# Performance work log

Measured on AMD Instinct MI355X. Metric: run time of the kernel, lower is better.

## Reference

```python
import jax, jax.numpy as jnp
import numpy as np

B, S, D, H = 4, 2048, 1024, 16
HD = D // H
THETA = 10000.0


def rope(x, pos, theta=THETA):
    # x: [..., seq, d], pos: broadcastable to [..., seq]
    d = x.shape[-1]
    half = d // 2
    inv_freq = 1.0 / (theta ** (jnp.arange(half, dtype=jnp.float32) * 2.0 / d))  # [half]
    ang = pos[..., None].astype(jnp.float32) * inv_freq  # [..., seq, half]
    cos, sin = jnp.cos(ang), jnp.sin(ang)
    x1, x2 = x[..., 0::2], x[..., 1::2]
    r1 = x1 * cos - x2 * sin
    r2 = x1 * sin + x2 * cos
    return jnp.stack([r1, r2], axis=-1).reshape(x.shape).astype(x.dtype)


def setup_inputs() -> dict:
    key = jax.random.key(0)
    ks = jax.random.split(key, 5)
    x = jax.random.normal(ks[0], (B, S, D), dtype=jnp.float32)
    token_positions = jnp.tile(jnp.arange(S, dtype=jnp.int64 if jax.config.jax_enable_x64 else jnp.int32), (B, 1))
    scale = 0.02
    Wq = jax.random.normal(ks[1], (D, D), dtype=jnp.float32) * scale
    Wk = jax.random.normal(ks[2], (D, D), dtype=jnp.float32) * scale
    Wv = jax.random.normal(ks[3], (D, D), dtype=jnp.float32) * scale
    Wo = jax.random.normal(ks[4], (D, D), dtype=jnp.float32) * scale
    return {"x": x, "token_positions": token_positions, "Wq": Wq, "Wk": Wk, "Wv": Wv, "Wo": Wo}


def reference(x, token_positions, Wq, Wk, Wv, Wo):
    b, s, d = x.shape
    # QKV projections (torch Linear: x @ W.T), split heads -> [b, h, s, hd]
    def proj(W):
        y = jnp.einsum('bsd,ed->bse', x, W)
        return y.reshape(b, s, H, HD).transpose(0, 2, 1, 3)
    Q, K, V = proj(Wq), proj(Wk), proj(Wv)
    # token_positions [..., seq] -> [..., 1, seq] to broadcast over heads
    pos = token_positions[:, None, :]  # [b, 1, s]
    Q = rope(Q, pos)
    K = rope(K, pos)
    # causal mask and scaled dot-product attention
    idx = jnp.arange(s)
    causal = idx[:, None] >= idx[None, :]  # [s, s], query >= key
    scores = jnp.einsum('bhqd,bhkd->bhqk', Q, K) / jnp.sqrt(jnp.float32(HD))
    scores = jnp.where(causal, scores, -jnp.inf)
    weights = jax.nn.softmax(scores, axis=-1)
    o = jnp.einsum('bhqk,bhkd->bhqd', weights, V)
    o = o.transpose(0, 2, 1, 3).reshape(b, s, d)  # merge heads
    return jnp.einsum('bsd,ed->bse', o, Wo)
```

## Files before the change

kernel.cpp:

```cpp
#include <hip/hip_runtime.h>

#define S_LEN 2048
#define NH 16
#define HDIM 64
#define DMODEL 1024

typedef __attribute__((ext_vector_type(8))) short bf16x8;
typedef __attribute__((ext_vector_type(4))) float f32x4;

__device__ __forceinline__ short f2bf(float f) {
    union { float f; unsigned u; } x; x.f = f;
    unsigned r = x.u + 0x7fffu + ((x.u >> 16) & 1u);
    return (short)(r >> 16);
}

#define GLDS(g, l) __builtin_amdgcn_global_load_lds( \
    (__attribute__((address_space(1))) void*)(g),    \
    (__attribute__((address_space(3))) void*)(l), 16, 0, 0)

#define QSCALE 0.18033688011112042f
#define FREQ_L 0.41524101186109327f

__global__ __launch_bounds__(256) void prep(const float* __restrict__ x,
                                            const float* __restrict__ wq,
                                            const float* __restrict__ wk,
                                            const float* __restrict__ wv,
                                            const float* __restrict__ wo,
                                            const int* __restrict__ tp,
                                            short* __restrict__ xb,
                                            short* __restrict__ wqb,
                                            short* __restrict__ wkb,
                                            short* __restrict__ wvb,
                                            short* __restrict__ wob,
                                            float2* __restrict__ tab) {
    int bid = blockIdx.x;
    if (bid < 8192) {
        int i = bid * 256 + threadIdx.x;
        float4 v = ((const float4*)x)[i];
        short4 o;
        o.x = f2bf(v.x); o.y = f2bf(v.y); o.z = f2bf(v.z); o.w = f2bf(v.w);
        ((short4*)xb)[i] = o;
    } else if (bid < 12288) {
        int sel = (bid - 8192) >> 10;
        const float* in = sel == 0 ? wq : sel == 1 ? wk : sel == 2 ? wv : wo;
        short* out = sel == 0 ? wqb : sel == 1 ? wkb : sel == 2 ? wvb : wob;
        int i = ((bid - 8192) & 1023) * 256 + threadIdx.x;
        float4 v = ((const float4*)in)[i];
        short4 o;
        o.x = f2bf(v.x); o.y = f2bf(v.y); o.z = f2bf(v.z); o.w = f2bf(v.w);
        ((short4*)out)[i] = o;
    } else {
        int idx = (bid - 12288) * 256 + threadIdx.x;
        int b = idx >> 16, s = (idx >> 5) & 2047, i = idx & 31;
        float p = (float)tp[(b << 11) + s];
        float freq = exp2f(-(float)i * FREQ_L);
        float sn, cs;
        sincosf(p * freq, &sn, &cs);
        tab[idx] = make_float2(cs, sn);
    }
}

__global__ __launch_bounds__(256) void gemm_qkv(const short* __restrict__ A,
                                                const short* __restrict__ Bq,
                                                const short* __restrict__ Bk,
                                                const short* __restrict__ Bv,
                                                const float2* __restrict__ tab,
                                                short* __restrict__ Qo,
                                                short* __restrict__ Ko,
                                                short* __restrict__ Vo) {
    constexpr int K = 1024, BK = 64;
    __shared__ __align__(16) short sa[128 * BK];
    __shared__ __align__(16) short sb[128 * BK];

    const int sel = blockIdx.x >> 3;
    const int bn = blockIdx.x & 7;
    const int bm = blockIdx.y;
    const short* Bm = sel == 0 ? Bq : sel == 1 ? Bk : Bv;
    short* Cb = sel == 0 ? Qo : sel == 1 ? Ko : Vo;

    const int tid = threadIdx.x;
    const int lane = tid & 63;
    const int w = tid >> 6;
    const int wm = w >> 1, wn = w & 1;
    const int quad = lane >> 4, l16 = lane & 15;
    const int l7 = l16 & 7;

    int aoff[4], boff[4];
#pragma unroll
    for (int i = 0; i < 4; i++) {
        int Lc = i * 256 + tid;
        int row = Lc >> 3;
        int cc = (Lc & 7) ^ (row & 7);
        aoff[i] = (bm * 128 + row) * K + cc * 8;
        boff[i] = (bn * 128 + row) * K + cc * 8;
    }

    f32x4 acc[4][4] = {};

    for (int k0 = 0; k0 < K; k0 += BK) {
#pragma unroll
        for (int i = 0; i < 4; i++)
            GLDS(A + aoff[i] + k0, (char*)sa + i * 4096 + w * 1024);
#pragma unroll
        for (int i = 0; i < 4; i++)
            GLDS(Bm + boff[i] + k0, (char*)sb + i * 4096 + w * 1024);
        __syncthreads();

#pragma unroll
        for (int kc = 0; kc < 2; kc++) {
            const int c = ((kc * 4 + quad) ^ l7) * 8;
            bf16x8 af[4], bfm[4];
#pragma unroll
            for (int mi = 0; mi < 4; mi++)
                af[mi] = *(const bf16x8*)&sa[(wm * 64 + mi * 16 + l16) * BK + c];
#pragma unroll
            for (int ni = 0; ni < 4; ni++)
                bfm[ni] = *(const bf16x8*)&sb[(wn * 64 + ni * 16 + l16) * BK + c];
#pragma unroll
            for (int mi = 0; mi < 4; mi++)
#pragma unroll
                for (int ni = 0; ni < 4; ni++)
                    acc[mi][ni] = __builtin_amdgcn_mfma_f32_16x16x32_bf16(af[mi], bfm[ni],
                                                                          acc[mi][ni], 0, 0, 0);
        }
        __syncthreads();
    }

    const int gm0 = bm * 128 + wm * 64;
    const int gn0 = bn * 128 + wn * 64;

    if (sel == 2) {
#pragma unroll
        for (int mi = 0; mi < 4; mi++)
#pragma unroll
            for (int ni = 0; ni < 4; ni++)
#pragma unroll
                for (int r = 0; r < 4; r++) {
                    int gm = gm0 + mi * 16 + quad * 4 + r;
                    int gn = gn0 + ni * 16 + l16;
                    int b = gm >> 11, s = gm & 2047;
                    int h = gn >> 6,  hd = gn & 63;
                    Cb[((b * NH + h) * HDIM + hd) * S_LEN + s] = f2bf(acc[mi][ni][r]);
                }
    } else {
        const float qs = (sel == 0) ? QSCALE : 1.0f;
#pragma unroll
        for (int mi = 0; mi < 4; mi++)
#pragma unroll
            for (int r = 0; r < 4; r++) {
                int gm = gm0 + mi * 16 + quad * 4 + r;
                const float2* trow = tab + (gm << 5);
                int b = gm >> 11, s = gm & 2047;
#pragma unroll
                for (int ni = 0; ni < 4; ni++) {
                    float2 cs = trow[ni * 8 + (l16 >> 1)];
                    float v = acc[mi][ni][r];
                    float prt = __shfl_xor(v, 1, 64);
                    float val = (l16 & 1) ? (prt * cs.y + v * cs.x)
                                          : (v * cs.x - prt * cs.y);
                    int gn = gn0 + ni * 16 + l16;
                    int h = gn >> 6, hd = gn & 63;
                    Cb[((b * NH + h) * S_LEN + s) * HDIM + hd] = f2bf(val * qs);
                }
            }
    }
}

__global__ __launch_bounds__(256) void gemm_o(const short* __restrict__ A,
                                              const short* __restrict__ Bm,
                                              float* __restrict__ Cf) {
    constexpr int N = 1024, K = 1024, BK = 64;
    __shared__ __align__(16) short sa[128 * BK];
    __shared__ __align__(16) short sb[64 * BK];

    const int tid = threadIdx.x;
    const int lane = tid & 63;
    const int w = tid >> 6;
    const int quad = lane >> 4, l16 = lane & 15;
    const int l7 = l16 & 7;
    const int bn = blockIdx.x, bm = blockIdx.y;
    const int arow0 = bm * 128, brow0 = bn * 64;

    int aoff[4], boff[2];
#pragma unroll
    for (int i = 0; i < 4; i++) {
        int Lc = i * 256 + tid;
        int row = Lc >> 3;
        int cc = (Lc & 7) ^ (row & 7);
        aoff[i] = (arow0 + row) * K + cc * 8;
    }
#pragma unroll
    for (int i = 0; i < 2; i++) {
        int Lc = i * 256 + tid;
        int row = Lc >> 3;
        int cc = (Lc & 7) ^ (row & 7);
        boff[i] = (brow0 + row) * K + cc * 8;
    }

    f32x4 acc[2][4] = {};

    for (int k0 = 0; k0 < K; k0 += BK) {
#pragma unroll
        for (int i = 0; i < 4; i++)
            GLDS(A + aoff[i] + k0, (char*)sa + i * 4096 + w * 1024);
#pragma unroll
        for (int i = 0; i < 2; i++)
            GLDS(Bm + boff[i] + k0, (char*)sb + i * 4096 + w * 1024);
        __syncthreads();

#pragma unroll
        for (int kc = 0; kc < 2; kc++) {
            const int c = ((kc * 4 + quad) ^ l7) * 8;
            bf16x8 af[2], bfm[4];
#pragma unroll
            for (int mi = 0; mi < 2; mi++)
                af[mi] = *(const bf16x8*)&sa[(w * 32 + mi * 16 + l16) * BK + c];
#pragma unroll
            for (int ni = 0; ni < 4; ni++)
                bfm[ni] = *(const bf16x8*)&sb[(ni * 16 + l16) * BK + c];
#pragma unroll
            for (int mi = 0; mi < 2; mi++)
#pragma unroll
                for (int ni = 0; ni < 4; ni++)
                    acc[mi][ni] = __builtin_amdgcn_mfma_f32_16x16x32_bf16(af[mi], bfm[ni],
                                                                          acc[mi][ni], 0, 0, 0);
        }
        __syncthreads();
    }

    const int gm0 = arow0 + w * 32;
#pragma unroll
    for (int mi = 0; mi < 2; mi++)
#pragma unroll
        for (int ni = 0; ni < 4; ni++)
#pragma unroll
            for (int r = 0; r < 4; r++) {
                int gm = gm0 + mi * 16 + quad * 4 + r;
                int gn = brow0 + ni * 16 + l16;
                Cf[gm * N + gn] = acc[mi][ni][r];
            }
}

__global__ __launch_bounds__(256, 3) void attn(const short* __restrict__ Q,
                                               const short* __restrict__ Km,
                                               const short* __restrict__ Vt,
                                               short* __restrict__ O) {
    __shared__ __align__(16) short kbuf[2][64 * 64];
    __shared__ __align__(16) short vbuf[2][64 * 64];
    __shared__ __align__(16) short pbuf[4][32 * 64];

    const int lane = threadIdx.x & 63;
    const int w = threadIdx.x >> 6;
    const int quad = lane >> 4, l16 = lane & 15;
    const int l7 = l16 & 7;
    const int bh = blockIdx.y;

    const short* Qg = Q  + bh * S_LEN * 64;
    const short* Kg = Km + bh * S_LEN * 64;
    const short* Vg = Vt + bh * 64 * S_LEN;
    short* myp = &pbuf[w][0];

    const int b = bh >> 4, h = bh & 15;

    bf16x8 ones;
#pragma unroll
    for (int j = 0; j < 8; j++) ones[j] = (short)0x3f80;

    auto stage = [&](int kt, int par) {
        const short* kt_base = Kg + kt * 64 * 64;
        const short* vt_base = Vg + kt * 64;
#pragma unroll
        for (int i = 0; i < 2; ++i) {
            int ch = w * 128 + i * 64 + lane;
            int row = ch >> 3;
            int c = (ch & 7) ^ (row & 7);
            GLDS(kt_base + row * 64 + c * 8, (char*)&kbuf[par][(w * 128 + i * 64) * 8]);
        }
#pragma unroll
        for (int i = 0; i < 2; ++i) {
            int ch = w * 128 + i * 64 + lane;
            int row = ch >> 3;
            int c = (ch & 7) ^ (row & 7);
            GLDS(vt_base + row * S_LEN + c * 8, (char*)&vbuf[par][(w * 128 + i * 64) * 8]);
        }
    };

    const int QtA = blockIdx.x;
    const int QtB = 15 - blockIdx.x;

    stage(0, 0);
    int t = 0;

    for (int phase = 0; phase < 2; ++phase) {
        const int Qt = phase ? QtB : QtA;
        const int nkt = 2 * Qt + 2;

        bf16x8 aq[2][2];
#pragma unroll
        for (int mi = 0; mi < 2; mi++) {
            int qrow = Qt * 128 + w * 32 + mi * 16 + l16;
#pragma unroll
            for (int kc = 0; kc < 2; kc++)
                aq[mi][kc] = *(const bf16x8*)&Qg[qrow * 64 + kc * 32 + quad * 8];
        }

        f32x4 oacc[2][4] = {};
        f32x4 lacc[2] = {};

        for (int kt = 0; kt < nkt; ++kt, ++t) {
            __syncthreads();
            if (kt + 1 < nkt)    stage(kt + 1, (t + 1) & 1);
            else if (phase == 0) stage(0,      (t + 1) & 1);
            const short* kb_cur = &kbuf[t & 1][0];
            const short* vb_cur = &vbuf[t & 1][0];

            f32x4 sc[2][4] = {};
#pragma unroll
            for (int nt = 0; nt < 4; nt++) {
                int raddr = (nt * 16 + l16) * 64;
#pragma unroll
                for (int kc = 0; kc < 2; kc++) {
                    bf16x8 kf = *(const bf16x8*)&kb_cur[raddr + (((quad + kc * 4) ^ l7) * 8)];
                    sc[0][nt] = __builtin_amdgcn_mfma_f32_16x16x32_bf16(aq[0][kc], kf, sc[0][nt], 0, 0, 0);
                    sc[1][nt] = __builtin_amdgcn_mfma_f32_16x16x32_bf16(aq[1][kc], kf, sc[1][nt], 0, 0, 0);
                }
            }
            if (kt >= nkt - 2) {
#pragma unroll
                for (int mi = 0; mi < 2; mi++)
#pragma unroll
                    for (int nt = 0; nt < 4; nt++)
#pragma unroll
                        for (int r = 0; r < 4; r++) {
                            int col = kt * 64 + nt * 16 + l16;
                            int row = Qt * 128 + w * 32 + mi * 16 + quad * 4 + r;
                            if (col > row) sc[mi][nt][r] = -__builtin_inff();
                        }
            }
#pragma unroll
            for (int mi = 0; mi < 2; mi++)
#pragma unroll
                for (int nt = 0; nt < 4; nt++)
#pragma unroll
                    for (int r = 0; r < 4; r++) {
                        float pv = __builtin_amdgcn_exp2f(sc[mi][nt][r]);
                        int q = mi * 16 + quad * 4 + r;
                        union { float f; unsigned short us[2]; } uu;
                        uu.f = pv;
                        myp[q * 64 + (((nt * 2 + (l16 >> 3)) ^ (q & 7)) * 8) + l7] =
                            (short)uu.us[1];
                    }
            bf16x8 ap[2][2];
#pragma unroll
            for (int mi = 0; mi < 2; mi++)
#pragma unroll
                for (int kc = 0; kc < 2; kc++)
                    ap[mi][kc] = *(const bf16x8*)&myp[(mi * 16 + l16) * 64 +
                                                      (((quad + kc * 4) ^ l7) * 8)];
#pragma unroll
            for (int nt = 0; nt < 4; nt++) {
                int raddr = (nt * 16 + l16) * 64;
#pragma unroll
                for (int kc = 0; kc < 2; kc++) {
                    bf16x8 vf = *(const bf16x8*)&vb_cur[raddr + (((quad + kc * 4) ^ l7) * 8)];
                    oacc[0][nt] = __builtin_amdgcn_mfma_f32_16x16x32_bf16(ap[0][kc], vf, oacc[0][nt], 0, 0, 0);
                    oacc[1][nt] = __builtin_amdgcn_mfma_f32_16x16x32_bf16(ap[1][kc], vf, oacc[1][nt], 0, 0, 0);
                }
            }
#pragma unroll
            for (int mi = 0; mi < 2; mi++) {
                lacc[mi] = __builtin_amdgcn_mfma_f32_16x16x32_bf16(ap[mi][0], ones, lacc[mi], 0, 0, 0);
                lacc[mi] = __builtin_amdgcn_mfma_f32_16x16x32_bf16(ap[mi][1], ones, lacc[mi], 0, 0, 0);
            }
        }
#pragma unroll
        for (int mi = 0; mi < 2; mi++)
#pragma unroll
            for (int r = 0; r < 4; r++) {
                float inv = 1.0f / lacc[mi][r];
                int srow = Qt * 128 + w * 32 + mi * 16 + quad * 4 + r;
#pragma unroll
                for (int nt = 0; nt < 4; nt++) {
                    int hd = nt * 16 + l16;
                    O[(b * S_LEN + srow) * DMODEL + h * HDIM + hd] = f2bf(oacc[mi][nt][r] * inv);
                }
            }
    }
}

extern "C" void kernel_launch(void* const* d_in, const int* in_sizes, int n_in,
                              void* d_out, int out_size, void* d_ws, size_t ws_size,
                              hipStream_t stream) {
    const float* x  = (const float*)d_in[0];
    const int*   tp = (const int*)d_in[1];
    const float* Wq = (const float*)d_in[2];
    const float* Wk = (const float*)d_in[3];
    const float* Wv = (const float*)d_in[4];
    const float* Wo = (const float*)d_in[5];
    float* out = (float*)d_out;

    char* ws = (char*)d_ws;
    const size_t MB = 1024 * 1024;
    short* xb  = (short*)(ws);
    short* wqb = (short*)(ws + 16 * MB);
    short* wkb = (short*)(ws + 18 * MB);
    short* wvb = (short*)(ws + 20 * MB);
    short* wob = (short*)(ws + 22 * MB);
    short* Qb  = (short*)(ws + 24 * MB);
    short* Kb  = (short*)(ws + 40 * MB);
    short* Vtb = (short*)(ws + 56 * MB);
    float2* tab = (float2*)d_out;

    prep<<<13312, 256, 0, stream>>>(x, Wq, Wk, Wv, Wo, tp,
                                    xb, wqb, wkb, wvb, wob, tab);

    gemm_qkv<<<dim3(24, 64), 256, 0, stream>>>(xb, wqb, wkb, wvb, tab, Qb, Kb, Vtb);

    attn<<<dim3(8, 64), 256, 0, stream>>>(Qb, Kb, Vtb, xb);

    gemm_o<<<dim3(16, 64), 256, 0, stream>>>(xb, wob, out);
}
```

Before: 279.4 us.

## Triple-buffer LDS in QKV and output-projection GEMMs with async prefetch pipeline

Both projection GEMMs switch from a single-buffered BK=64 loop with two __syncthreads per step to a three-stage ring of BK=32 LDS tiles. Global-to-LDS loads for tile k+2 are issued before computing tile k, and completion is tracked with explicit vmcnt waits and a single barrier per step. The LDS swizzle is adjusted for the narrower tile. This is meant to overlap global memory latency with MFMA work and halve the barriers per tile. The cost is more LDS per block and reliance on hand-tuned vmcnt counts for correctness.

New measurement: 276.0 us. About the same (-1.2%).

```diff
diff --git a/kernel.cpp b/kernel.cpp
--- a/kernel.cpp
+++ b/kernel.cpp
@@ -68,9 +68,9 @@
                                                 short* __restrict__ Qo,
                                                 short* __restrict__ Ko,
                                                 short* __restrict__ Vo) {
-    constexpr int K = 1024, BK = 64;
-    __shared__ __align__(16) short sa[128 * BK];
-    __shared__ __align__(16) short sb[128 * BK];
+    constexpr int K = 1024, BK = 32;
+    __shared__ __align__(16) short sa[3][128 * BK];
+    __shared__ __align__(16) short sb[3][128 * BK];
 
     const int sel = blockIdx.x >> 3;
     const int bn = blockIdx.x & 7;
@@ -83,48 +83,69 @@
     const int w = tid >> 6;
     const int wm = w >> 1, wn = w & 1;
     const int quad = lane >> 4, l16 = lane & 15;
-    const int l7 = l16 & 7;
-
-    int aoff[4], boff[4];
-#pragma unroll
-    for (int i = 0; i < 4; i++) {
-        int Lc = i * 256 + tid;
-        int row = Lc >> 3;
-        int cc = (Lc & 7) ^ (row & 7);
-        aoff[i] = (bm * 128 + row) * K + cc * 8;
-        boff[i] = (bn * 128 + row) * K + cc * 8;
-    }
+
+    int aoff[2], boff[2];
+#pragma unroll
+    for (int i = 0; i < 2; i++) {
+        int cs = i * 256 + tid;
+        int row = cs >> 2;
+        int gc = (cs & 3) ^ ((row >> 1) & 3);
+        aoff[i] = (bm * 128 + row) * K + gc * 8;
+        boff[i] = (bn * 128 + row) * K + gc * 8;
+    }
+
+    auto stage = [&](int kt, int b) {
+        const int k0 = kt * BK;
+#pragma unroll
+        for (int i = 0; i < 2; i++)
+            GLDS(A + aoff[i] + k0, (char*)&sa[b][0] + i * 4096 + w * 1024);
+#pragma unroll
+        for (int i = 0; i < 2; i++)
+            GLDS(Bm + boff[i] + k0, (char*)&sb[b][0] + i * 4096 + w * 1024);
+    };
 
     f32x4 acc[4][4] = {};
-
-    for (int k0 = 0; k0 < K; k0 += BK) {
-#pragma unroll
-        for (int i = 0; i < 4; i++)
-            GLDS(A + aoff[i] + k0, (char*)sa + i * 4096 + w * 1024);
-#pragma unroll
-        for (int i = 0; i < 4; i++)
-            GLDS(Bm + boff[i] + k0, (char*)sb + i * 4096 + w * 1024);
-        __syncthreads();
-
-#pragma unroll
-        for (int kc = 0; kc < 2; kc++) {
-            const int c = ((kc * 4 + quad) ^ l7) * 8;
-            bf16x8 af[4], bfm[4];
+    const int rsw = (quad ^ ((l16 >> 1) & 3)) * 8;
+
+    auto compute = [&](int b) {
+        bf16x8 af[4];
+#pragma unroll
+        for (int mi = 0; mi < 4; mi++)
+            af[mi] = *(const bf16x8*)&sa[b][(wm * 64 + mi * 16 + l16) * BK + rsw];
+#pragma unroll
+        for (int ni = 0; ni < 4; ni++) {
+            bf16x8 bfr = *(const bf16x8*)&sb[b][(wn * 64 + ni * 16 + l16) * BK + rsw];
 #pragma unroll
             for (int mi = 0; mi < 4; mi++)
-                af[mi] = *(const bf16x8*)&sa[(wm * 64 + mi * 16 + l16) * BK + c];
-#pragma unroll
-            for (int ni = 0; ni < 4; ni++)
-                bfm[ni] = *(const bf16x8*)&sb[(wn * 64 + ni * 16 + l16) * BK + c];
-#pragma unroll
-            for (int mi = 0; mi < 4; mi++)
-#pragma unroll
-                for (int ni = 0; ni < 4; ni++)
-                    acc[mi][ni] = __builtin_amdgcn_mfma_f32_16x16x32_bf16(af[mi], bfm[ni],
-                                                                          acc[mi][ni], 0, 0, 0);
-        }
-        __syncthreads();
-    }
+                acc[mi][ni] = __builtin_amdgcn_mfma_f32_16x16x32_bf16(af[mi], bfr,
+                                                                     acc[mi][ni], 0, 0, 0);
+        }
+    };
+
+    stage(0, 0);
+    stage(1, 1);
+
+    auto step = [&](int kt, int b, int bs) {
+        asm volatile("s_waitcnt vmcnt(4)" ::: "memory");
+        __builtin_amdgcn_s_barrier();
+        __builtin_amdgcn_sched_barrier(0);
+        stage(kt + 2, bs);
+        compute(b);
+    };
+
+    for (int kt = 0; kt < 30; kt += 3) {
+        step(kt + 0, 0, 2);
+        step(kt + 1, 1, 0);
+        step(kt + 2, 2, 1);
+    }
+    asm volatile("s_waitcnt vmcnt(4)" ::: "memory");
+    __builtin_amdgcn_s_barrier();
+    __builtin_amdgcn_sched_barrier(0);
+    compute(0);
+    asm volatile("s_waitcnt vmcnt(0)" ::: "memory");
+    __builtin_amdgcn_s_barrier();
+    __builtin_amdgcn_sched_barrier(0);
+    compute(1);
 
     const int gm0 = bm * 128 + wm * 64;
     const int gn0 = bn * 128 + wn * 64;
@@ -167,66 +188,83 @@
 }
 
 __global__ __launch_bounds__(256) void gemm_o(const short* __restrict__ A,
-                                              const short* __restrict__ Bm,
+                                              const short* __restrict__ Bw,
                                               float* __restrict__ Cf) {
-    constexpr int N = 1024, K = 1024, BK = 64;
-    __shared__ __align__(16) short sa[128 * BK];
-    __shared__ __align__(16) short sb[64 * BK];
+    constexpr int N = 1024, K = 1024, BK = 32;
+    __shared__ __align__(16) short sa[3][128 * BK];
+    __shared__ __align__(16) short sb[3][64 * BK];
 
     const int tid = threadIdx.x;
     const int lane = tid & 63;
     const int w = tid >> 6;
     const int quad = lane >> 4, l16 = lane & 15;
-    const int l7 = l16 & 7;
     const int bn = blockIdx.x, bm = blockIdx.y;
     const int arow0 = bm * 128, brow0 = bn * 64;
 
-    int aoff[4], boff[2];
-#pragma unroll
-    for (int i = 0; i < 4; i++) {
-        int Lc = i * 256 + tid;
-        int row = Lc >> 3;
-        int cc = (Lc & 7) ^ (row & 7);
-        aoff[i] = (arow0 + row) * K + cc * 8;
-    }
+    int aoff[2], boff;
 #pragma unroll
     for (int i = 0; i < 2; i++) {
-        int Lc = i * 256 + tid;
-        int row = Lc >> 3;
-        int cc = (Lc & 7) ^ (row & 7);
-        boff[i] = (brow0 + row) * K + cc * 8;
-    }
+        int cs = i * 256 + tid;
+        int row = cs >> 2;
+        int gc = (cs & 3) ^ ((row >> 1) & 3);
+        aoff[i] = (arow0 + row) * K + gc * 8;
+    }
+    {
+        int row = tid >> 2;
+        int gc = (tid & 3) ^ ((row >> 1) & 3);
+        boff = (brow0 + row) * K + gc * 8;
+    }
+
+    auto stage = [&](int kt, int b) {
+        const int k0 = kt * BK;
+#pragma unroll
+        for (int i = 0; i < 2; i++)
+            GLDS(A + aoff[i] + k0, (char*)&sa[b][0] + i * 4096 + w * 1024);
+        GLDS(Bw + boff + k0, (char*)&sb[b][0] + w * 1024);
+    };
 
     f32x4 acc[2][4] = {};
-
-    for (int k0 = 0; k0 < K; k0 += BK) {
-#pragma unroll
-        for (int i = 0; i < 4; i++)
-            GLDS(A + aoff[i] + k0, (char*)sa + i * 4096 + w * 1024);
-#pragma unroll
-        for (int i = 0; i < 2; i++)
-            GLDS(Bm + boff[i] + k0, (char*)sb + i * 4096 + w * 1024);
-        __syncthreads();
-
-#pragma unroll
-        for (int kc = 0; kc < 2; kc++) {
-            const int c = ((kc * 4 + quad) ^ l7) * 8;
-            bf16x8 af[2], bfm[4];
+    const int rsw = (quad ^ ((l16 >> 1) & 3)) * 8;
+
+    auto compute = [&](int b) {
+        bf16x8 af[2];
+#pragma unroll
+        for (int mi = 0; mi < 2; mi++)
+            af[mi] = *(const bf16x8*)&sa[b][(w * 32 + mi * 16 + l16) * BK + rsw];
+#pragma unroll
+        for (int ni = 0; ni < 4; ni++) {
+            bf16x8 bfr = *(const bf16x8*)&sb[b][(ni * 16 + l16) * BK + rsw];
 #pragma unroll
             for (int mi = 0; mi < 2; mi++)
-                af[mi] = *(const bf16x8*)&sa[(w * 32 + mi * 16 + l16) * BK + c];
-#pragma unroll
-            for (int ni = 0; ni < 4; ni++)
-                bfm[ni] = *(const bf16x8*)&sb[(ni * 16 + l16) * BK + c];
-#pragma unroll
-            for (int mi = 0; mi < 2; mi++)
-#pragma unroll
-                for (int ni = 0; ni < 4; ni++)
-                    acc[mi][ni] = __builtin_amdgcn_mfma_f32_16x16x32_bf16(af[mi], bfm[ni],
-                                                                          acc[mi][ni], 0, 0, 0);
-        }
-        __syncthreads();
-    }
+                acc[mi][ni] = __builtin_amdgcn_mfma_f32_16x16x32_bf16(af[mi], bfr,
+                                                                     acc[mi][ni], 0, 0, 0);
+        }
+    };
+
+    stage(0, 0);
+    stage(1, 1);
+
+    auto step = [&](int kt, int b, int bs) {
+        asm volatile("s_waitcnt vmcnt(3)" ::: "memory");
+        __builtin_amdgcn_s_barrier();
+        __builtin_amdgcn_sched_barrier(0);
+        stage(kt + 2, bs);
+        compute(b);
+    };
+
+    for (int kt = 0; kt < 30; kt += 3) {
+        step(kt + 0, 0, 2);
+        step(kt + 1, 1, 0);
+        step(kt + 2, 2, 1);
+    }
+    asm volatile("s_waitcnt vmcnt(3)" ::: "memory");
+    __builtin_amdgcn_s_barrier();
+    __builtin_amdgcn_sched_barrier(0);
+    compute(0);
+    asm volatile("s_waitcnt vmcnt(0)" ::: "memory");
+    __builtin_amdgcn_s_barrier();
+    __builtin_amdgcn_sched_barrier(0);
+    compute(1);
 
     const int gm0 = arow0 + w * 32;
 #pragma unroll
```
